# Kernel tuning notes

Hardware: AMD Instinct MI355X
Metric: run time of the kernel (lower is better)

The kernel has to match this reference:

```python
import jax, jax.numpy as jnp
import numpy as np
from jax import lax

B, T = 2, 2048
D = 512        # d_model
K = 64         # k_lookback (causal window)


def setup_inputs() -> dict:
    key = jax.random.key(0)
    k1, k2, k3 = jax.random.split(key, 3)
    x = jax.random.normal(k1, (B, 1, T), jnp.float32)
    conv_w = jax.random.normal(k2, (D, 1, 3), jnp.float32) * 0.2
    conv_b = jax.random.normal(k3, (D,), jnp.float32) * 0.05
    gate = jnp.array(0.5, jnp.float32)  # nn.Parameter scalar
    return {"x": x, "conv_w": conv_w, "conv_b": conv_b, "gate": gate}


def reference(x, conv_w, conv_b, gate):
    # feature_proj: Conv1d(1, D, k=3, pad=1) + exact GELU (dropout inactive at eval)
    q = lax.conv_general_dilated(
        x, conv_w, window_strides=(1,), padding=[(1, 1)],
        dimension_numbers=("NCH", "OIH", "NCH"))
    q = jax.nn.gelu(q + conv_b[None, :, None], approximate=False)  # [B, D, T]

    # causal sliding windows: keys_windows[b,c,t,j] = q[b,c, t-(K-1)+j] (0 outside)
    padded = jnp.pad(q, ((0, 0), (0, 0), (K - 1, 0)))
    idx = jnp.arange(T)[:, None] + jnp.arange(K)[None, :]  # [T, K]
    kw = padded[:, :, idx]                                  # [B, D, T, K]

    energy = jnp.einsum("bct,bctk->btk", q, kw)             # [B, T, K]
    attn = jax.nn.softmax(energy / np.float32(np.sqrt(D)), axis=-1)
    context = jnp.einsum("btk,bctk->bct", attn, kw)         # [B, D, T]
    return context * jnp.tanh(gate)
```

## Files before the change

kernel.cpp:

```cpp
#include <hip/hip_runtime.h>
#include <math.h>

#define B 2
#define T 2048
#define D 512
#define KW 64
#define SCALE 0.044194173824159216f

#define RQ (64 + T + 16)
#define TTP (64 + T + 16)

typedef __attribute__((ext_vector_type(8))) short short8;
typedef __attribute__((ext_vector_type(4))) float f32x4;

__device__ __forceinline__ ushort f2bf(float f) {
  union { float f; unsigned u; } v; v.f = f;
  unsigned r = v.u + 0x7fffu + ((v.u >> 16) & 1u);
  return (ushort)(r >> 16);
}

__global__ __launch_bounds__(256) void k_conv(
    const float* __restrict__ x, const float* __restrict__ w,
    const float* __restrict__ bias, ushort* __restrict__ q,
    ushort* __restrict__ qT) {
  int blk = blockIdx.x;
  int tid = threadIdx.x;

  if (blk >= 512) {
    int ztid = (blk - 512) * 256 + tid;
    const uint4 z = {0u, 0u, 0u, 0u};
    for (int task = ztid; task < 20480; task += 2048) {
      size_t e;
      if (task < 8192) {
        int b = task >> 12, i = task & 4095;
        e = (size_t)b * RQ * D + (size_t)i * 8;
      } else if (task < 10240) {
        int idx = task - 8192;
        int b = idx >> 10, i = idx & 1023;
        e = (size_t)b * RQ * D + (size_t)(64 + T) * D + (size_t)i * 8;
      } else if (task < 18432) {
        int idx = task - 10240;
        int r = idx >> 3, i = idx & 7;
        e = (size_t)r * TTP + (size_t)i * 8;
        *(uint4*)(qT + e) = z;
        continue;
      } else {
        int idx = task - 18432;
        int r = idx >> 1, i = idx & 1;
        e = (size_t)r * TTP + 64 + T + (size_t)i * 8;
        *(uint4*)(qT + e) = z;
        continue;
      }
      *(uint4*)(q + e) = z;
    }
    return;
  }

  __shared__ float s_tile[64 * 65];
  int b   = blk >> 8;
  int rem = blk & 255;
  int t0  = (rem >> 3) << 6;
  int c0  = (rem & 7) << 6;

  int lt = tid >> 2;
  int cb = (tid & 3) << 4;
  int t = t0 + lt;
  float xm1 = (t > 0)     ? x[b * T + t - 1] : 0.f;
  float x0  =               x[b * T + t];
  float xp1 = (t < T - 1) ? x[b * T + t + 1] : 0.f;
#pragma unroll
  for (int e = 0; e < 16; ++e) {
    int c = c0 + cb + e;
    float v = xm1 * w[c * 3] + x0 * w[c * 3 + 1] + xp1 * w[c * 3 + 2] + bias[c];
    float g = 0.5f * v * (1.f + erff(v * 0.70710678118654752f));
    q[((size_t)b * RQ + 64 + t) * D + c] = f2bf(g);
    s_tile[lt * 65 + cb + e] = g;
  }
  __syncthreads();

  int lc = tid >> 2;
  int tb = (tid & 3) << 4;
#pragma unroll
  for (int e = 0; e < 16; ++e) {
    int ltt = tb + e;
    qT[((size_t)b * D + c0 + lc) * TTP + 64 + t0 + ltt] =
        f2bf(s_tile[ltt * 65 + lc]);
  }
}

__global__ __launch_bounds__(256) void k_attn(
    const ushort* __restrict__ q, const ushort* __restrict__ qT,
    const float* __restrict__ gate, float* __restrict__ out) {
  __shared__ float s_E[4 * 5 * 4 * 64];
  __shared__ alignas(16) ushort s_attn[4][16 * 96];

  int blk  = blockIdx.x;
  int tile = (blk & 7) * 32 + (blk >> 3);
  int b  = tile >> 7;
  int t0 = (tile & 127) << 4;
  int tid  = threadIdx.x;
  int wv   = tid >> 6;
  int lane = tid & 63;
  int n    = lane & 15;
  int quad = lane >> 4;

  const ushort* qb = q + (size_t)b * RQ * D + (size_t)64 * D;
  const ushort* qTb = qT + (size_t)b * D * TTP;

  short8 afr[4], bfr[4][5];
#pragma unroll
  for (int i = 0; i < 4; ++i) {
    int cofs = (wv * 4 + i) * 32 + quad * 8;
    afr[i] = *(const short8*)(qb + (size_t)(t0 + n) * D + cofs);
#pragma unroll
    for (int jc = 0; jc < 5; ++jc) {
      int tp = t0 - (KW - 1) + jc * 16 + n;
      bfr[i][jc] = *(const short8*)(qb + (ptrdiff_t)tp * D + cofs);
    }
  }

  f32x4 acc[5];
#pragma unroll
  for (int jc = 0; jc < 5; ++jc) acc[jc] = (f32x4){0.f, 0.f, 0.f, 0.f};
#pragma unroll
  for (int i = 0; i < 4; ++i)
#pragma unroll
    for (int jc = 0; jc < 5; ++jc)
      acc[jc] = __builtin_amdgcn_mfma_f32_16x16x32_bf16(afr[i], bfr[i][jc],
                                                        acc[jc], 0, 0, 0);

#pragma unroll
  for (int jc = 0; jc < 5; ++jc)
#pragma unroll
    for (int r = 0; r < 4; ++r)
      s_E[((wv * 5 + jc) * 4 + r) * 64 + lane] = acc[jc][r];
  __syncthreads();

#pragma unroll
  for (int ww = 0; ww < 4; ++ww) {
    if (ww == wv) continue;
#pragma unroll
    for (int jc = 0; jc < 5; ++jc)
#pragma unroll
      for (int r = 0; r < 4; ++r)
        acc[jc][r] += s_E[((ww * 5 + jc) * 4 + r) * 64 + lane];
  }

  ushort* sa = s_attn[wv];
#pragma unroll
  for (int r = 0; r < 4; ++r) {
    int m = quad * 4 + r;
    float e[5];
    float mx = -1e30f;
#pragma unroll
    for (int jc = 0; jc < 5; ++jc) {
      int j = jc * 16 + n;
      bool valid = (j >= m) && (j <= m + (KW - 1));
      e[jc] = valid ? acc[jc][r] * SCALE : -1e30f;
      mx = fmaxf(mx, e[jc]);
    }
#pragma unroll
    for (int off = 1; off <= 8; off <<= 1) mx = fmaxf(mx, __shfl_xor(mx, off, 64));
    float p[5];
    float s = 0.f;
#pragma unroll
    for (int jc = 0; jc < 5; ++jc) {
      p[jc] = (e[jc] > -1e29f) ? __expf(e[jc] - mx) : 0.f;
      s += p[jc];
    }
#pragma unroll
    for (int off = 1; off <= 8; off <<= 1) s += __shfl_xor(s, off, 64);
    float inv = 1.f / s;
#pragma unroll
    for (int jc = 0; jc < 5; ++jc) {
      int j = jc * 16 + n;
      sa[m * 96 + j + 1] = f2bf(p[jc] * inv);
    }
    int jp = (n == 0) ? 0 : (80 + n);
    sa[m * 96 + jp] = 0;
  }

  short8 afr2[3];
#pragma unroll
  for (int ks = 0; ks < 3; ++ks)
    afr2[ks] = *(const short8*)(sa + n * 96 + ks * 32 + quad * 8);

  short8 bfr2[8][3];
#pragma unroll
  for (int ncl = 0; ncl < 8; ++ncl) {
    int c = (wv * 8 + ncl) * 16 + n;
#pragma unroll
    for (int ks = 0; ks < 3; ++ks) {
      bfr2[ncl][ks] = *(const short8*)(qTb + (size_t)c * TTP + t0 + ks * 32 + quad * 8);
    }
  }

  const float tg = tanhf(gate[0]);
#pragma unroll
  for (int ncl = 0; ncl < 8; ++ncl) {
    int c = (wv * 8 + ncl) * 16 + n;
    f32x4 co = (f32x4){0.f, 0.f, 0.f, 0.f};
#pragma unroll
    for (int ks = 0; ks < 3; ++ks)
      co = __builtin_amdgcn_mfma_f32_16x16x32_bf16(afr2[ks], bfr2[ncl][ks],
                                                   co, 0, 0, 0);
    f32x4 o;
    o[0] = co[0] * tg; o[1] = co[1] * tg; o[2] = co[2] * tg; o[3] = co[3] * tg;
    *(f32x4*)(out + ((size_t)b * D + c) * T + t0 + quad * 4) = o;
  }
}

extern "C" void kernel_launch(void* const* d_in, const int* in_sizes, int n_in,
                              void* d_out, int out_size, void* d_ws, size_t ws_size,
                              hipStream_t stream) {
  const float* x      = (const float*)d_in[0];
  const float* conv_w = (const float*)d_in[1];
  const float* conv_b = (const float*)d_in[2];
  const float* gate   = (const float*)d_in[3];
  float* out = (float*)d_out;

  ushort* q_ws  = (ushort*)d_ws;
  ushort* qT_ws = q_ws + (size_t)B * RQ * D;

  k_conv<<<520, 256, 0, stream>>>(x, conv_w, conv_b, q_ws, qT_ws);
  k_attn<<<B * T / 16, 256, 0, stream>>>(q_ws, qT_ws, gate, out);
}
```

Measured before the change: 79.67 us.

## Vectorize conv stores, remap conv blocks per XCD, prefetch qT fragments early

Measured after the change: 77.88 us. 1.02x faster.

```diff
diff --git a/kernel.cpp b/kernel.cpp
--- a/kernel.cpp
+++ b/kernel.cpp
@@ -57,10 +57,12 @@
   }
 
   __shared__ float s_tile[64 * 65];
-  int b   = blk >> 8;
-  int rem = blk & 255;
-  int t0  = (rem >> 3) << 6;
-  int c0  = (rem & 7) << 6;
+
+  int xcd = blk & 7;
+  int i   = blk >> 3;
+  int b   = xcd >> 2;
+  int t0  = (xcd & 3) * 512 + (i >> 3) * 64;
+  int c0  = (i & 7) * 64;
 
   int lt = tid >> 2;
   int cb = (tid & 3) << 4;
@@ -68,27 +70,39 @@
   float xm1 = (t > 0)     ? x[b * T + t - 1] : 0.f;
   float x0  =               x[b * T + t];
   float xp1 = (t < T - 1) ? x[b * T + t + 1] : 0.f;
+  short8 h0, h1;
 #pragma unroll
   for (int e = 0; e < 16; ++e) {
     int c = c0 + cb + e;
     float v = xm1 * w[c * 3] + x0 * w[c * 3 + 1] + xp1 * w[c * 3 + 2] + bias[c];
     float g = 0.5f * v * (1.f + erff(v * 0.70710678118654752f));
-    q[((size_t)b * RQ + 64 + t) * D + c] = f2bf(g);
     s_tile[lt * 65 + cb + e] = g;
+    if (e < 8) h0[e] = (short)f2bf(g); else h1[e - 8] = (short)f2bf(g);
+  }
+  {
+    ushort* qp = q + ((size_t)b * RQ + 64 + t) * D + c0 + cb;
+    *(short8*)qp = h0;
+    *(short8*)(qp + 8) = h1;
   }
   __syncthreads();
 
   int lc = tid >> 2;
   int tb = (tid & 3) << 4;
-#pragma unroll
-  for (int e = 0; e < 16; ++e) {
-    int ltt = tb + e;
-    qT[((size_t)b * D + c0 + lc) * TTP + 64 + t0 + ltt] =
-        f2bf(s_tile[ltt * 65 + lc]);
-  }
-}
-
-__global__ __launch_bounds__(256) void k_attn(
+  short8 v0, v1;
+#pragma unroll
+  for (int e = 0; e < 8; ++e)
+    v0[e] = (short)f2bf(s_tile[(tb + e) * 65 + lc]);
+#pragma unroll
+  for (int e = 0; e < 8; ++e)
+    v1[e] = (short)f2bf(s_tile[(tb + 8 + e) * 65 + lc]);
+  {
+    ushort* qp = qT + ((size_t)b * D + c0 + lc) * TTP + 64 + t0 + tb;
+    *(short8*)qp = v0;
+    *(short8*)(qp + 8) = v1;
+  }
+}
+
+__global__ __launch_bounds__(256, 1) void k_attn(
     const ushort* __restrict__ q, const ushort* __restrict__ qT,
     const float* __restrict__ gate, float* __restrict__ out) {
   __shared__ float s_E[4 * 5 * 4 * 64];
@@ -118,6 +132,15 @@
       bfr[i][jc] = *(const short8*)(qb + (ptrdiff_t)tp * D + cofs);
     }
   }
+  short8 bfr2[8][3];
+#pragma unroll
+  for (int ncl = 0; ncl < 8; ++ncl) {
+    int c = (wv * 8 + ncl) * 16 + n;
+#pragma unroll
+    for (int ks = 0; ks < 3; ++ks)
+      bfr2[ncl][ks] =
+          *(const short8*)(qTb + (size_t)c * TTP + t0 + ks * 32 + quad * 8);
+  }
 
   f32x4 acc[5];
 #pragma unroll
@@ -184,16 +207,6 @@
 #pragma unroll
   for (int ks = 0; ks < 3; ++ks)
     afr2[ks] = *(const short8*)(sa + n * 96 + ks * 32 + quad * 8);
-
-  short8 bfr2[8][3];
-#pragma unroll
-  for (int ncl = 0; ncl < 8; ++ncl) {
-    int c = (wv * 8 + ncl) * 16 + n;
-#pragma unroll
-    for (int ks = 0; ks < 3; ++ks) {
-      bfr2[ncl][ks] = *(const short8*)(qTb + (size_t)c * TTP + t0 + ks * 32 + quad * 8);
-    }
-  }
 
   const float tg = tanhf(gate[0]);
 #pragma unroll
```
